# Optimization experiments

Measured on AMD Instinct MI355X. Metric: run time of the kernel, lower is better.

## Reference

```python
import jax, jax.numpy as jnp
import numpy as np

SEQ_LEN, BATCH, INPUT_SIZE = 2048, 16, 1024
HIDDEN_SIZE = 1024  # must equal INPUT_SIZE (source uses input[t] as highway residual)
NUM_MATRICES = 3


def setup_inputs() -> dict:
    key = jax.random.key(0)
    k_in, k_w, k_b, k_v = jax.random.split(key, 4)
    val_range = (3.0 / INPUT_SIZE) ** 0.5
    inp = {
        "input": jax.random.normal(k_in, (SEQ_LEN, BATCH, INPUT_SIZE), dtype=jnp.float32),
        "weight": jax.random.uniform(k_w, (INPUT_SIZE, HIDDEN_SIZE * NUM_MATRICES),
                                     minval=-val_range, maxval=val_range, dtype=jnp.float32),
        # reset_parameters zeroes bias/v; use small random values so the gating is non-trivial
        "bias": jax.random.normal(k_b, (2 * HIDDEN_SIZE,), dtype=jnp.float32) * 0.1,
        "v": jax.random.normal(k_v, (2 * HIDDEN_SIZE,), dtype=jnp.float32) * 0.1,
    }
    return inp


def reference(input, weight, bias, v):
    seq_len, batch, input_size = input.shape
    hidden = HIDDEN_SIZE
    # One big matmul up-front: [S,B,I] @ [I,3H] -> [S,B,H,3]
    U = (input @ weight).reshape(seq_len, batch, hidden, NUM_MATRICES)
    U0, U1, U2 = U[..., 0], U[..., 1], U[..., 2]
    b0, b1 = bias.reshape(2, hidden)
    # Source quirk: v0, v1 are (erroneously) taken from bias, not v. Preserve it.
    v0, v1 = bias.reshape(2, hidden)

    c0 = jnp.zeros((batch, hidden), dtype=input.dtype)

    def step(c_prev, xs):
        u0, u1, u2, x_t = xs
        f_t = jax.nn.sigmoid(u0 + v0 * c_prev + b0)
        r_t = jax.nn.sigmoid(u1 + v1 * c_prev + b1)
        c_t = f_t * c_prev + (1.0 - f_t) * u2
        h_t = r_t * c_t + (1.0 - r_t) * x_t
        return c_t, (h_t, c_t)

    _, (H, C) = jax.lax.scan(step, c0, (U0, U1, U2, input))
    return H, C
```

## Files before the change

### kernel.cpp

```cpp
#include <hip/hip_runtime.h>
#include <hip/hip_bf16.h>
#include <stdint.h>
#include <stddef.h>

#define SEQ 2048
#define BATCH 16
#define HID 1024
#define MM (SEQ*BATCH)
#define NN (3*HID)
#define KK HID

typedef __bf16 bf16x8 __attribute__((ext_vector_type(8)));
typedef float floatx4 __attribute__((ext_vector_type(4)));

template <typename UT> __device__ inline void storeU(UT* p, float v);
template <> __device__ inline void storeU<float>(float* p, float v) { *p = v; }
template <> __device__ inline void storeU<__bf16>(__bf16* p, float v) { *p = (__bf16)v; }
template <typename UT> __device__ inline float loadU(const UT* p);
template <> __device__ inline float loadU<float>(const float* p) { return *p; }
template <> __device__ inline float loadU<__bf16>(const __bf16* p) { return (float)*p; }

__global__ __launch_bounds__(256) void cast_a_kernel(const float* __restrict__ in,
                                                     __bf16* __restrict__ out) {
  size_t i = (size_t)blockIdx.x * 256 + threadIdx.x;
  float4 v = ((const float4*)in)[i];
  typedef __bf16 bf16x4 __attribute__((ext_vector_type(4)));
  bf16x4 o;
  o[0] = (__bf16)v.x; o[1] = (__bf16)v.y; o[2] = (__bf16)v.z; o[3] = (__bf16)v.w;
  ((bf16x4*)out)[i] = o;
}

__global__ __launch_bounds__(256) void pack_w_kernel(const float* __restrict__ w,
                                                     __bf16* __restrict__ wp) {
  __shared__ float tile[32][33];
  int n0 = blockIdx.x * 32, k0 = blockIdx.y * 32;
  int tx = threadIdx.x, ty = threadIdx.y;
#pragma unroll
  for (int r = 0; r < 4; r++)
    tile[ty + 8*r][tx] = w[(size_t)(k0 + ty + 8*r) * NN + n0 + tx];
  __syncthreads();
#pragma unroll
  for (int r = 0; r < 4; r++)
    wp[(size_t)(n0 + ty + 8*r) * KK + k0 + tx] = (__bf16)tile[tx][ty + 8*r];
}

template <typename UT>
__global__ __launch_bounds__(256) void gemm_kernel(const __bf16* __restrict__ A,
                                                   const __bf16* __restrict__ B,
                                                   UT* __restrict__ U) {
  __shared__ __align__(16) char smem[32768];
  const int tid  = threadIdx.x;
  const int lane = tid & 63;
  const int wave = tid >> 6;
  const int tileN = blockIdx.x * 128;
  const int tileM = blockIdx.y * 128;

  const char* gsrc[8];
  uint32_t    ldsoff[8];
#pragma unroll
  for (int j = 0; j < 8; j++) {
    int s   = j * 256 + tid;
    int isB = s >> 10;
    int s2  = s & 1023;
    int row = s2 >> 3;
    int cs  = s2 & 7;
    int kc  = cs ^ (row & 7);
    const __bf16* base = isB ? (B + (size_t)(tileN + row) * KK)
                             : (A + (size_t)(tileM + row) * KK);
    gsrc[j]   = (const char*)(base + kc * 8);
    ldsoff[j] = (uint32_t)(j * 4096 + wave * 1024);
  }

  const int wm = (wave >> 1) * 64;
  const int wn = (wave & 1) * 64;
  const int g  = lane >> 4;

  uint32_t aoff[4], boff[4];
#pragma unroll
  for (int i = 0; i < 4; i++) {
    int row  = wm + i * 16 + (lane & 15);
    aoff[i]  = (uint32_t)((row * 8 + (g ^ (row & 7))) * 16);
    int nrow = wn + i * 16 + (lane & 15);
    boff[i]  = (uint32_t)(16384 + (nrow * 8 + (g ^ (nrow & 7))) * 16);
  }

  floatx4 acc[4][4];
#pragma unroll
  for (int mi = 0; mi < 4; mi++)
#pragma unroll
    for (int ni = 0; ni < 4; ni++) acc[mi][ni] = (floatx4)0.0f;

  for (int it = 0; it < KK / 64; ++it) {
    __syncthreads();
#pragma unroll
    for (int j = 0; j < 8; j++)
      __builtin_amdgcn_global_load_lds(
          (const __attribute__((address_space(1))) void*)(gsrc[j]),
          (__attribute__((address_space(3))) void*)(smem + ldsoff[j]), 16, 0, 0);
#pragma unroll
    for (int j = 0; j < 8; j++) gsrc[j] += 128;
    __syncthreads();

#pragma unroll
    for (int ks = 0; ks < 2; ++ks) {
      bf16x8 a[4], b[4];
#pragma unroll
      for (int i = 0; i < 4; i++) {
        a[i] = *(const bf16x8*)(smem + (aoff[i] ^ (ks * 64)));
        b[i] = *(const bf16x8*)(smem + (boff[i] ^ (ks * 64)));
      }
#pragma unroll
      for (int mi = 0; mi < 4; mi++)
#pragma unroll
        for (int ni = 0; ni < 4; ni++)
          acc[mi][ni] = __builtin_amdgcn_mfma_f32_16x16x32_bf16(
              a[mi], b[ni], acc[mi][ni], 0, 0, 0);
    }
  }

  const int r0 = (lane >> 4) * 4;
  const int cc = lane & 15;
#pragma unroll
  for (int mi = 0; mi < 4; mi++)
#pragma unroll
    for (int ni = 0; ni < 4; ni++) {
      int col = tileN + wn + ni * 16 + cc;
#pragma unroll
      for (int r = 0; r < 4; r++) {
        int row = tileM + wm + mi * 16 + r0 + r;
        storeU(&U[(size_t)row * NN + col], acc[mi][ni][r]);
      }
    }
}

__device__ inline float sigmoidf_fast(float z) {
  return __builtin_amdgcn_rcpf(1.0f + __expf(-z));
}

template <typename UT>
__global__ __launch_bounds__(64) void scan_kernel(const UT* __restrict__ U,
                                                  const float* __restrict__ x,
                                                  const float* __restrict__ bias,
                                                  float* __restrict__ out) {
  int idx = blockIdx.x * 64 + threadIdx.x;
  int b = idx >> 10, h = idx & 1023;
  float b0 = bias[h], b1 = bias[HID + h];

  const UT*    up = U + (size_t)b * NN + 3 * h;
  const float* xp = x + idx;
  float* Hout = out + idx;
  float* Cout = out + (size_t)SEQ * BATCH * HID + idx;

  constexpr int P = 16;
  float pu0[P], pu1[P], pu2[P], px[P];
#pragma unroll
  for (int i = 0; i < P; i++) {
    const UT* u = up + (size_t)i * (BATCH * NN);
    pu0[i] = loadU(u); pu1[i] = loadU(u + 1); pu2[i] = loadU(u + 2);
    px[i]  = xp[(size_t)i * (BATCH * HID)];
  }

  float c = 0.0f;
  int tt = 0;
  for (; tt < SEQ - P; tt += P) {
#pragma unroll
    for (int i = 0; i < P; i++) {
      int t = tt + i;
      float u0 = pu0[i], u1 = pu1[i], u2 = pu2[i], xv = px[i];
      const UT* u = up + (size_t)(t + P) * (BATCH * NN);
      pu0[i] = loadU(u); pu1[i] = loadU(u + 1); pu2[i] = loadU(u + 2);
      px[i]  = xp[(size_t)(t + P) * (BATCH * HID)];

      float f = sigmoidf_fast(u0 + b0 * c + b0);
      float r = sigmoidf_fast(u1 + b1 * c + b1);
      c = f * c + (1.0f - f) * u2;
      float ht = r * c + (1.0f - r) * xv;
      Cout[(size_t)t * (BATCH * HID)] = c;
      Hout[(size_t)t * (BATCH * HID)] = ht;
    }
  }
#pragma unroll
  for (int i = 0; i < P; i++) {
    int t = tt + i;
    float f = sigmoidf_fast(pu0[i] + b0 * c + b0);
    float r = sigmoidf_fast(pu1[i] + b1 * c + b1);
    c = f * c + (1.0f - f) * pu2[i];
    float ht = r * c + (1.0f - r) * px[i];
    Cout[(size_t)t * (BATCH * HID)] = c;
    Hout[(size_t)t * (BATCH * HID)] = ht;
  }
}

extern "C" void kernel_launch(void* const* d_in, const int* in_sizes, int n_in,
                              void* d_out, int out_size, void* d_ws, size_t ws_size,
                              hipStream_t stream) {
  const float* input  = (const float*)d_in[0];
  const float* weight = (const float*)d_in[1];
  const float* bias   = (const float*)d_in[2];
  float* out = (float*)d_out;

  char* ws = (char*)d_ws;
  const size_t apB = (size_t)MM * KK * 2;
  const size_t wpB = (size_t)NN * KK * 2;
  const size_t uF  = (size_t)MM * NN * 4;
  bool useF32 = ws_size >= uF + apB + wpB;
  size_t uB = useF32 ? uF : uF / 2;

  void*   Uv = (void*)ws;
  __bf16* Ap = (__bf16*)(ws + uB);
  __bf16* Wp = (__bf16*)(ws + uB + apB);

  cast_a_kernel<<<(MM * KK) / 4 / 256, 256, 0, stream>>>(input, Ap);
  pack_w_kernel<<<dim3(NN / 32, KK / 32), dim3(32, 8), 0, stream>>>(weight, Wp);

  if (useF32) {
    gemm_kernel<float><<<dim3(NN / 128, MM / 128), 256, 0, stream>>>(Ap, Wp, (float*)Uv);
    scan_kernel<float><<<(BATCH * HID) / 64, 64, 0, stream>>>((const float*)Uv, input, bias, out);
  } else {
    gemm_kernel<__bf16><<<dim3(NN / 128, MM / 128), 256, 0, stream>>>(Ap, Wp, (__bf16*)Uv);
    scan_kernel<__bf16><<<(BATCH * HID) / 64, 64, 0, stream>>>((const __bf16*)Uv, input, bias, out);
  }
}
```

Measured before the change: 856.8 us.

## Add producer-consumer LDS-staged scan kernel and remap GEMM block order

Adds a scan kernel in which three producer waves stream chunks of U and x into double-buffered LDS with global_load_lds, while one consumer wave runs the sequential recurrence from LDS. This targets the global-load latency on the serial dependency chain in the old register-prefetch scan. Separately, it remaps GEMM block indices into eight interleaved groups to change the order tiles are scheduled, likely for cache or XCD locality. The new scan uses only one compute wave per block, and the LDS buffer size limits occupancy.

```diff
diff --git a/kernel.cpp b/kernel.cpp
--- a/kernel.cpp
+++ b/kernel.cpp
@@ -52,8 +52,11 @@
   const int tid  = threadIdx.x;
   const int lane = tid & 63;
   const int wave = tid >> 6;
-  const int tileN = blockIdx.x * 128;
-  const int tileM = blockIdx.y * 128;
+
+  const int bid = blockIdx.y * (NN / 128) + blockIdx.x;
+  const int nid = (bid & 7) * ((MM / 128) * (NN / 128) / 8) + (bid >> 3);
+  const int tileN = (nid % (NN / 128)) * 128;
+  const int tileM = (nid / (NN / 128)) * 128;
 
   const char* gsrc[8];
   uint32_t    ldsoff[8];
@@ -137,6 +140,66 @@
   return __builtin_amdgcn_rcpf(1.0f + __expf(-z));
 }
 
+#define SCH 32
+
+__global__ __launch_bounds__(256) void scan_pc_kernel(const float* __restrict__ U,
+                                                      const float* __restrict__ x,
+                                                      const float* __restrict__ bias,
+                                                      float* __restrict__ out) {
+  __shared__ __align__(16) char smem[2 * SCH * 1024];
+  const int tid  = threadIdx.x;
+  const int wave = tid >> 6;
+  const int lane = tid & 63;
+  const int b    = blockIdx.x >> 4;
+  const int h0   = (blockIdx.x & 15) * 64;
+
+  const char* const ub = (const char*)(U + (size_t)b * NN + 3 * h0);
+  const char* const xb = (const char*)(x + (size_t)b * HID + h0);
+
+  float b0 = 0.f, b1 = 0.f, c = 0.f;
+  if (wave == 0) { b0 = bias[h0 + lane]; b1 = bias[HID + h0 + lane]; }
+
+  auto issue = [&](int ci) {
+    char* dst = smem + (ci & 1) * (SCH * 1024);
+    for (int s = wave - 1; s < SCH; s += 3) {
+      size_t t = (size_t)ci * SCH + s;
+      const char* us = ub + t * (size_t)(BATCH * NN * 4);
+      const char* xs = xb + t * (size_t)(BATCH * HID * 4);
+      const char* src = (lane < 48) ? (us + lane * 16) : (xs + (lane - 48) * 16);
+      __builtin_amdgcn_global_load_lds(
+          (const __attribute__((address_space(1))) void*)src,
+          (__attribute__((address_space(3))) void*)(dst + s * 1024), 16, 0, 0);
+    }
+  };
+
+  if (wave > 0) issue(0);
+  __syncthreads();
+
+  for (int ci = 0; ci < SEQ / SCH; ++ci) {
+    if (wave > 0) {
+      if (ci + 1 < SEQ / SCH) issue(ci + 1);
+    } else {
+      const float* buf = (const float*)(smem + (ci & 1) * (SCH * 1024));
+#pragma unroll 4
+      for (int s = 0; s < SCH; ++s) {
+        const float* p = buf + s * 256;
+        float u0 = p[3 * lane];
+        float u1 = p[3 * lane + 1];
+        float u2 = p[3 * lane + 2];
+        float xv = p[192 + lane];
+        float f = sigmoidf_fast(u0 + b0 * c + b0);
+        float r = sigmoidf_fast(u1 + b1 * c + b1);
+        c = f * c + (1.0f - f) * u2;
+        float ht = r * c + (1.0f - r) * xv;
+        size_t o = (size_t)(ci * SCH + s) * (BATCH * HID) + (b * HID + h0 + lane);
+        out[o] = ht;
+        out[(size_t)SEQ * BATCH * HID + o] = c;
+      }
+    }
+    __syncthreads();
+  }
+}
+
 template <typename UT>
 __global__ __launch_bounds__(64) void scan_kernel(const UT* __restrict__ U,
                                                   const float* __restrict__ x,
@@ -215,7 +278,7 @@
 
   if (useF32) {
     gemm_kernel<float><<<dim3(NN / 128, MM / 128), 256, 0, stream>>>(Ap, Wp, (float*)Uv);
-    scan_kernel<float><<<(BATCH * HID) / 64, 64, 0, stream>>>((const float*)Uv, input, bias, out);
+    scan_pc_kernel<<<BATCH * 16, 256, 0, stream>>>((const float*)Uv, input, bias, out);
   } else {
     gemm_kernel<__bf16><<<dim3(NN / 128, MM / 128), 256, 0, stream>>>(Ap, Wp, (__bf16*)Uv);
     scan_kernel<__bf16><<<(BATCH * HID) / 64, 64, 0, stream>>>((const __bf16*)Uv, input, bias, out);
```

After: 788.8 us. 1.09x faster.
